# Performance work log

Measured on AMD Instinct MI355X. Metric: run time of the kernel, lower is better.

## Reference

```python
import jax, jax.numpy as jnp
import numpy as np

# Conv2D_DT config (matches init_kwargs)
IN_C = 64
OUT_C = 128
K = (3, 3)
STRIDE = (1, 1)
PAD = (1, 1)
DIL = (1, 1)
INPUT_DIM = K[0] * K[1] * IN_C  # 576


def setup_inputs() -> dict:
    key = jax.random.key(0)
    k1, k2 = jax.random.split(key)
    x = jax.random.normal(k1, (32, IN_C, 56, 56), dtype=jnp.float32)
    # DistanceTransform centroids: one INPUT_DIM-dim center per output channel
    W = jax.random.normal(k2, (OUT_C, INPUT_DIM), dtype=jnp.float32) * (1.0 / np.sqrt(INPUT_DIM))
    return {"x": x, "W": W}


def _unfold_patches(x):
    # Equivalent of nn.Unfold: output [N, C*kH*kW, oH, oW], feature dim ordered
    # (channel, kh, kw) — matches torch.nn.Unfold ordering.
    return jax.lax.conv_general_dilated_patches(
        x,
        filter_shape=K,
        window_strides=STRIDE,
        padding=[(PAD[0], PAD[0]), (PAD[1], PAD[1])],
        rhs_dilation=DIL,
        dimension_numbers=("NCHW", "OIHW", "NCHW"),
    )


def reference(x, W):
    # patches: [N, D, oH, oW] with D = C*kH*kW
    patches = _unfold_patches(x)
    # Euclidean (p=2) distance between every patch and every centroid, via the
    # expanded quadratic form (the compute-heavy cross term is a GEMM):
    # ||p - w||^2 = ||p||^2 + ||w||^2 - 2 p.w
    x2 = jnp.sum(patches * patches, axis=1)            # [N, oH, oW]
    w2 = jnp.sum(W * W, axis=1)                        # [O]
    cross = jnp.einsum("ndhw,od->nohw", patches, W)    # [N, O, oH, oW]
    d2 = x2[:, None] + w2[None, :, None, None] - 2.0 * cross
    dist = jnp.sqrt(jnp.maximum(d2, 0.0))              # [N, O, oH, oW]
    return dist
```

## Files before the change

### kernel.cpp

```cpp
#include <hip/hip_runtime.h>
#include <hip/hip_bf16.h>
#include <stdint.h>
#include <math.h>

#define NIMG 32
#define CIN 64
#define HWD 56
#define OCH 128
#define PH 58

typedef __attribute__((ext_vector_type(8))) short bfrag;
typedef __attribute__((ext_vector_type(4))) float facc;
typedef __attribute__((ext_vector_type(8))) unsigned short u16x8;

__device__ __forceinline__ unsigned short f2bf(float f) {
  union { float f; uint32_t u; } a; a.f = f;
  uint32_t u = a.u;
  return (unsigned short)((u + 0x7FFFu + ((u >> 16) & 1u)) >> 16);
}

__device__ __forceinline__ void gload_lds16(const void* g, void* l) {
  __builtin_amdgcn_global_load_lds(
      (const __attribute__((address_space(1))) unsigned int*)g,
      (__attribute__((address_space(3))) unsigned int*)l, 16, 0, 0);
}

__global__ __launch_bounds__(256) void k_prep_x(const float* __restrict__ x,
                                                unsigned short* __restrict__ xh,
                                                float* __restrict__ s) {
  const int n = blockIdx.x / HWD, h = blockIdx.x % HWD;
  __shared__ float xt[CIN][HWD + 1];
  const float* xp = x + ((size_t)n * CIN * HWD + h) * HWD;
  for (int i = threadIdx.x; i < CIN * HWD; i += 256) {
    int c = i / HWD, ww = i % HWD;
    xt[c][ww] = xp[(size_t)c * HWD * HWD + ww];
  }
  __syncthreads();
  const size_t rowbase = ((size_t)(n * PH + h + 1) * PH + 1) * CIN;
  for (int t = threadIdx.x; t < HWD * 8; t += 256) {
    int ww = t >> 3, seg = t & 7;
    u16x8 v;
#pragma unroll
    for (int j = 0; j < 8; ++j) v[j] = f2bf(xt[seg * 8 + j][ww]);
    *(u16x8*)(xh + rowbase + (size_t)ww * CIN + seg * 8) = v;
  }
  for (int ww = threadIdx.x; ww < HWD; ww += 256) {
    float acc = 0.f;
#pragma unroll
    for (int c = 0; c < CIN; ++c) { float v = xt[c][ww]; acc += v * v; }
    s[((size_t)n * HWD + h) * HWD + ww] = acc;
  }
  if (threadIdx.x < 16) {
    int ww = (threadIdx.x >> 3) ? (PH - 1) : 0, seg = threadIdx.x & 7;
    u16x8 z = {0, 0, 0, 0, 0, 0, 0, 0};
    *(u16x8*)(xh + ((size_t)(n * PH + h + 1) * PH + ww) * CIN + seg * 8) = z;
  }
  if (h == 0) {
    u16x8 z = {0, 0, 0, 0, 0, 0, 0, 0};
    for (int t = threadIdx.x; t < 2 * PH * 8; t += 256) {
      int r = (t >= PH * 8) ? (PH - 1) : 0;
      int rem = t % (PH * 8);
      int ww = rem >> 3, seg = rem & 7;
      *(u16x8*)(xh + ((size_t)(n * PH + r) * PH + ww) * CIN + seg * 8) = z;
    }
  }
}

__global__ __launch_bounds__(256) void k_aux(const float* __restrict__ s,
                                             float* __restrict__ x2,
                                             const float* __restrict__ W,
                                             unsigned short* __restrict__ Wt,
                                             float* __restrict__ w2) {
  if (blockIdx.x < 392) {
    int i = blockIdx.x * 256 + threadIdx.x;
    if (i >= NIMG * HWD * HWD) return;
    int n = i / (HWD * HWD), r = i % (HWD * HWD), oh = r / HWD, ow = r % HWD;
    const float* sp = s + (size_t)n * HWD * HWD;
    float acc = 0.f;
#pragma unroll
    for (int dh = -1; dh <= 1; ++dh) {
      int hh = oh + dh;
      if ((unsigned)hh >= HWD) continue;
#pragma unroll
      for (int dw = -1; dw <= 1; ++dw) {
        int wwp = ow + dw;
        if ((unsigned)wwp >= HWD) continue;
        acc += sp[hh * HWD + wwp];
      }
    }
    x2[i] = acc;
  } else {
    if (threadIdx.x >= 64) return;
    int o = blockIdx.x - 392, c = threadIdx.x;
    float sum = 0.f;
#pragma unroll
    for (int kp = 0; kp < 9; ++kp) {
      float v = W[o * 576 + c * 9 + kp];
      sum += v * v;
      Wt[(size_t)kp * (OCH * CIN) + o * CIN + c] = f2bf(v);
    }
#pragma unroll
    for (int off = 32; off; off >>= 1) sum += __shfl_down(sum, off);
    if (c == 0) w2[o] = sum;
  }
}

__global__ __launch_bounds__(256, 2) void k_main(
    const unsigned short* __restrict__ xh, const unsigned short* __restrict__ Wt,
    const float* __restrict__ x2, const float* __restrict__ w2,
    float* __restrict__ out) {
  __shared__ __align__(16) unsigned short slab[352 * 64];
  const int bid = blockIdx.x;
  const int n = bid / 14, band = bid % 14;
  const int oh0 = band * 4;
  const int tid = threadIdx.x, wv = tid >> 6, lane = tid & 63;

  {
    const int seg = lane & 7, r8 = lane >> 3;
    for (int i = wv; i < 44; i += 4) {
      int row = i * 8 + r8;
      int re = row < 348 ? row : 347;
      int lseg = seg ^ (re & 7);
      int dr = re / 58, pc = re % 58;
      const unsigned short* src =
          xh + ((size_t)(n * PH + oh0 + dr) * PH + pc) * CIN + lseg * 8;
      gload_lds16(src, (char*)slab + i * 1024);
    }
  }
  __syncthreads();

  const int lane15 = lane & 15, q = lane >> 4, q16 = q * 16;
  const int wm = wv >> 1, wn = wv & 1;

  int srow0[7];
#pragma unroll
  for (int mf = 0; mf < 7; ++mf) {
    int pl = wm * 112 + mf * 16 + lane15;
    srow0[mf] = (pl / 56) * 58 + (pl % 56);
  }
  int boff[4];
#pragma unroll
  for (int nf = 0; nf < 4; ++nf)
    boff[nf] = (wn * 64 + nf * 16 + lane15) * CIN + q * 8;

  const char* slabb = (const char*)slab;

  auto load_b = [&](bfrag* dst, int ks) {
    const unsigned short* wp = Wt + (size_t)(ks >> 1) * (OCH * CIN) + (ks & 1) * 32;
#pragma unroll
    for (int nf = 0; nf < 4; ++nf) dst[nf] = *(const bfrag*)(wp + boff[nf]);
  };
  auto load_a = [&](bfrag* dst, int ks) {
    const int kp = ks >> 1, cbyte = (ks & 1) * 64 + q16;
    const int rof = (kp / 3) * 58 + (kp % 3);
#pragma unroll
    for (int mf = 0; mf < 7; ++mf) {
      int srow = srow0[mf] + rof;
      dst[mf] = *(const bfrag*)(slabb + srow * 128 + (cbyte ^ ((srow & 7) << 4)));
    }
  };

  facc acc[7][4] = {};
  bfrag a[2][7], b[2][4];
  load_b(b[0], 0);
  load_a(a[0], 0);
#pragma unroll
  for (int ks = 0; ks < 18; ++ks) {
    const int cur = ks & 1, nxt = cur ^ 1;
    if (ks < 17) {
      load_b(b[nxt], ks + 1);
      load_a(a[nxt], ks + 1);
    }
#pragma unroll
    for (int nf = 0; nf < 4; ++nf)
#pragma unroll
      for (int mf = 0; mf < 7; ++mf)
        acc[mf][nf] = __builtin_amdgcn_mfma_f32_16x16x32_bf16(a[cur][mf], b[cur][nf],
                                                              acc[mf][nf], 0, 0, 0);
  }

#pragma unroll
  for (int mf = 0; mf < 7; ++mf) {
    int mb = wm * 112 + mf * 16 + q * 4;
    int oh = oh0 + mb / 56, ow = mb % 56;
    facc xv = *(const facc*)(x2 + ((size_t)n * HWD + oh) * HWD + ow);
#pragma unroll
    for (int nf = 0; nf < 4; ++nf) {
      int o = wn * 64 + nf * 16 + lane15;
      float w2o = w2[o];
      facc d;
#pragma unroll
      for (int r = 0; r < 4; ++r) {
        float v = xv[r] + w2o - 2.0f * acc[mf][nf][r];
        d[r] = sqrtf(v > 0.f ? v : 0.f);
      }
      *(facc*)(out + (((size_t)n * OCH + o) * HWD + oh) * HWD + ow) = d;
    }
  }
}

extern "C" void kernel_launch(void* const* d_in, const int* in_sizes, int n_in,
                              void* d_out, int out_size, void* d_ws, size_t ws_size,
                              hipStream_t stream) {
  const float* x = (const float*)d_in[0];
  const float* W = (const float*)d_in[1];
  float* out = (float*)d_out;
  char* ws = (char*)d_ws;

  unsigned short* xh = (unsigned short*)ws;
  float* s = (float*)(ws + 13778944);
  float* x2 = (float*)(ws + 13778944 + 401408);
  unsigned short* Wt = (unsigned short*)(ws + 13778944 + 802816);
  float* w2 = (float*)(ws + 13778944 + 802816 + 147456);

  k_prep_x<<<dim3(NIMG * HWD), dim3(256), 0, stream>>>(x, xh, s);
  k_aux<<<dim3(392 + OCH), dim3(256), 0, stream>>>(s, x2, W, Wt, w2);
  k_main<<<dim3(NIMG * 14), dim3(256), 0, stream>>>(xh, Wt, x2, w2, out);
}
```

Baseline: 120.5 us.

## Split output channels across two blocks and batch four rows in prep kernel

The main GEMM kernel now splits the 128 output channels into two halves per band. That doubles the grid to 896 blocks. A bid remap spreads consecutive workgroups across XCDs, and occupancy is raised to 3 blocks per CU. The A fragments are no longer double-buffered, while B gets a triple-buffered prefetch. The prep kernel processes four rows per block with float4 loads and a transposed LDS tile, which fuses the bf16 conversion with the squared-norm sum. The goal is better CU utilization and fewer small blocks, at the cost of loading each input slab twice and losing A-load latency hiding.

```diff
diff --git a/kernel.cpp b/kernel.cpp
--- a/kernel.cpp
+++ b/kernel.cpp
@@ -25,43 +25,56 @@
       (__attribute__((address_space(3))) unsigned int*)l, 16, 0, 0);
 }
 
-__global__ __launch_bounds__(256) void k_prep_x(const float* __restrict__ x,
-                                                unsigned short* __restrict__ xh,
-                                                float* __restrict__ s) {
-  const int n = blockIdx.x / HWD, h = blockIdx.x % HWD;
-  __shared__ float xt[CIN][HWD + 1];
-  const float* xp = x + ((size_t)n * CIN * HWD + h) * HWD;
-  for (int i = threadIdx.x; i < CIN * HWD; i += 256) {
-    int c = i / HWD, ww = i % HWD;
-    xt[c][ww] = xp[(size_t)c * HWD * HWD + ww];
+__global__ __launch_bounds__(256, 2) void k_prep_x(const float* __restrict__ x,
+                                                   unsigned short* __restrict__ xh,
+                                                   float* __restrict__ s) {
+  const int n = blockIdx.x / 14, h4 = blockIdx.x % 14;
+  __shared__ float lt[224][65];
+  const int tid = threadIdx.x;
+  const float* xp = x + ((size_t)n * CIN * HWD + h4 * 4) * HWD;
+#pragma unroll
+  for (int i = 0; i < 14; ++i) {
+    int idx = tid + i * 256;
+    int c = idx / 56, j = idx % 56;
+    int row = j / 14, col = (j % 14) * 4;
+    float4 v = *(const float4*)(xp + (size_t)c * (HWD * HWD) + row * HWD + col);
+    int pix = row * 56 + col;
+    lt[pix + 0][c] = v.x; lt[pix + 1][c] = v.y;
+    lt[pix + 2][c] = v.z; lt[pix + 3][c] = v.w;
   }
   __syncthreads();
-  const size_t rowbase = ((size_t)(n * PH + h + 1) * PH + 1) * CIN;
-  for (int t = threadIdx.x; t < HWD * 8; t += 256) {
-    int ww = t >> 3, seg = t & 7;
-    u16x8 v;
-#pragma unroll
-    for (int j = 0; j < 8; ++j) v[j] = f2bf(xt[seg * 8 + j][ww]);
-    *(u16x8*)(xh + rowbase + (size_t)ww * CIN + seg * 8) = v;
-  }
-  for (int ww = threadIdx.x; ww < HWD; ww += 256) {
-    float acc = 0.f;
-#pragma unroll
-    for (int c = 0; c < CIN; ++c) { float v = xt[c][ww]; acc += v * v; }
-    s[((size_t)n * HWD + h) * HWD + ww] = acc;
-  }
-  if (threadIdx.x < 16) {
-    int ww = (threadIdx.x >> 3) ? (PH - 1) : 0, seg = threadIdx.x & 7;
+  if (tid < 224) {
+    int r = tid / 56, w = tid % 56;
+    int h = h4 * 4 + r;
+    float sum = 0.f;
+    const size_t gb = ((size_t)(n * PH + h + 1) * PH + (w + 1)) * CIN;
+#pragma unroll
+    for (int seg = 0; seg < 8; ++seg) {
+      u16x8 v;
+#pragma unroll
+      for (int k = 0; k < 8; ++k) {
+        float f = lt[tid][seg * 8 + k];
+        sum += f * f;
+        v[k] = f2bf(f);
+      }
+      *(u16x8*)(xh + gb + seg * 8) = v;
+    }
+    s[((size_t)n * HWD + h) * HWD + w] = sum;
+  }
+  if (tid >= 224 && tid < 224 + 64) {
+    int t = tid - 224;
+    int r = t >> 4, side = (t >> 3) & 1, seg = t & 7;
+    int ww = side ? (PH - 1) : 0;
     u16x8 z = {0, 0, 0, 0, 0, 0, 0, 0};
-    *(u16x8*)(xh + ((size_t)(n * PH + h + 1) * PH + ww) * CIN + seg * 8) = z;
-  }
-  if (h == 0) {
+    *(u16x8*)(xh + ((size_t)(n * PH + h4 * 4 + r + 1) * PH + ww) * CIN + seg * 8) = z;
+  }
+  if (h4 == 0) {
     u16x8 z = {0, 0, 0, 0, 0, 0, 0, 0};
-    for (int t = threadIdx.x; t < 2 * PH * 8; t += 256) {
-      int r = (t >= PH * 8) ? (PH - 1) : 0;
+    for (int t = tid; t < 2 * PH * 8; t += 256) {
+      int rr = (t >= PH * 8) ? (PH - 1) : 0;
       int rem = t % (PH * 8);
       int ww = rem >> 3, seg = rem & 7;
-      *(u16x8*)(xh + ((size_t)(n * PH + r) * PH + ww) * CIN + seg * 8) = z;
+      *(u16x8*)(xh + ((size_t)(n * PH + rr) * PH + ww) * CIN + seg * 8) = z;
     }
   }
 }
@@ -105,14 +118,15 @@
   }
 }
 
-__global__ __launch_bounds__(256, 2) void k_main(
+__global__ __launch_bounds__(256, 3) void k_main(
     const unsigned short* __restrict__ xh, const unsigned short* __restrict__ Wt,
     const float* __restrict__ x2, const float* __restrict__ w2,
     float* __restrict__ out) {
   __shared__ __align__(16) unsigned short slab[352 * 64];
   const int bid = blockIdx.x;
-  const int n = bid / 14, band = bid % 14;
-  const int oh0 = band * 4;
+  const int wgid = (bid & 7) * 112 + (bid >> 3);
+  const int band = wgid >> 1, nh = wgid & 1;
+  const int n = band / 14, oh0 = (band % 14) * 4;
   const int tid = threadIdx.x, wv = tid >> 6, lane = tid & 63;
 
   {
@@ -138,17 +152,17 @@
     int pl = wm * 112 + mf * 16 + lane15;
     srow0[mf] = (pl / 56) * 58 + (pl % 56);
   }
-  int boff[4];
-#pragma unroll
-  for (int nf = 0; nf < 4; ++nf)
-    boff[nf] = (wn * 64 + nf * 16 + lane15) * CIN + q * 8;
+  int boff[2];
+#pragma unroll
+  for (int nf = 0; nf < 2; ++nf)
+    boff[nf] = (nh * 64 + wn * 32 + nf * 16 + lane15) * CIN + q * 8;
 
   const char* slabb = (const char*)slab;
 
   auto load_b = [&](bfrag* dst, int ks) {
     const unsigned short* wp = Wt + (size_t)(ks >> 1) * (OCH * CIN) + (ks & 1) * 32;
 #pragma unroll
-    for (int nf = 0; nf < 4; ++nf) dst[nf] = *(const bfrag*)(wp + boff[nf]);
+    for (int nf = 0; nf < 2; ++nf) dst[nf] = *(const bfrag*)(wp + boff[nf]);
   };
   auto load_a = [&](bfrag* dst, int ks) {
     const int kp = ks >> 1, cbyte = (ks & 1) * 64 + q16;
@@ -160,22 +174,20 @@
     }
   };
 
-  facc acc[7][4] = {};
-  bfrag a[2][7], b[2][4];
+  facc acc[7][2] = {};
+  bfrag a[7], b[3][2];
   load_b(b[0], 0);
-  load_a(a[0], 0);
+  load_b(b[1], 1);
 #pragma unroll
   for (int ks = 0; ks < 18; ++ks) {
-    const int cur = ks & 1, nxt = cur ^ 1;
-    if (ks < 17) {
-      load_b(b[nxt], ks + 1);
-      load_a(a[nxt], ks + 1);
-    }
-#pragma unroll
-    for (int nf = 0; nf < 4; ++nf)
+    load_a(a, ks);
+    if (ks < 16) load_b(b[(ks + 2) % 3], ks + 2);
+    const int cb = ks % 3;
+#pragma unroll
+    for (int nf = 0; nf < 2; ++nf)
 #pragma unroll
       for (int mf = 0; mf < 7; ++mf)
-        acc[mf][nf] = __builtin_amdgcn_mfma_f32_16x16x32_bf16(a[cur][mf], b[cur][nf],
+        acc[mf][nf] = __builtin_amdgcn_mfma_f32_16x16x32_bf16(a[mf], b[cb][nf],
                                                               acc[mf][nf], 0, 0, 0);
   }
 
@@ -185,8 +197,8 @@
     int oh = oh0 + mb / 56, ow = mb % 56;
     facc xv = *(const facc*)(x2 + ((size_t)n * HWD + oh) * HWD + ow);
 #pragma unroll
-    for (int nf = 0; nf < 4; ++nf) {
-      int o = wn * 64 + nf * 16 + lane15;
+    for (int nf = 0; nf < 2; ++nf) {
+      int o = nh * 64 + wn * 32 + nf * 16 + lane15;
       float w2o = w2[o];
       facc d;
 #pragma unroll
@@ -213,7 +225,7 @@
   unsigned short* Wt = (unsigned short*)(ws + 13778944 + 802816);
   float* w2 = (float*)(ws + 13778944 + 802816 + 147456);
 
-  k_prep_x<<<dim3(NIMG * HWD), dim3(256), 0, stream>>>(x, xh, s);
+  k_prep_x<<<dim3(NIMG * 14), dim3(256), 0, stream>>>(x, xh, s);
   k_aux<<<dim3(392 + OCH), dim3(256), 0, stream>>>(s, x2, W, Wt, w2);
-  k_main<<<dim3(NIMG * 14), dim3(256), 0, stream>>>(xh, Wt, x2, w2, out);
-}
+  k_main<<<dim3(NIMG * 28), dim3(256), 0, stream>>>(xh, Wt, x2, w2, out);
+}
```

New measurement: 119.7 us. No clear change (-0.6%).
